# Kernel tuning notes

Hardware: AMD Instinct MI355X
Metric: run time of the kernel (lower is better)

Reference implementation:

```python
import jax, jax.numpy as jnp
import numpy as np

H, C_K, C_Q = 4, 512, 512


def setup_inputs() -> dict:
    key = jax.random.key(0)
    ks = jax.random.split(key, 6)
    s = 1.0 / np.sqrt(512.0)
    return {
        "x_k": jax.random.normal(ks[0], (4096, 512), jnp.float32),
        "x_q": jax.random.normal(ks[1], (4096, 512), jnp.float32),
        "k_w": jax.random.normal(ks[2], (H * C_K, 512), jnp.float32) * s,
        "q_w": jax.random.normal(ks[3], (H * C_Q, 512), jnp.float32) * s,
        "attn_w": jax.random.normal(ks[4], (H, C_K, C_Q), jnp.float32) * s,
        "proj_w": jax.random.normal(ks[5], (C_K, C_Q), jnp.float32) * s,
    }


def reference(x_k, x_q, k_w, q_w, attn_w, proj_w):
    # Project keys/queries and split into heads: [H, N, c]
    xk = (x_k @ k_w.T).reshape(-1, H, C_K).transpose(1, 0, 2)
    xq = (x_q @ q_w.T).reshape(-1, H, C_Q).transpose(1, 0, 2)
    # Bilinear scores: alphas[h, n, m] = xk[h,n,:] @ attn_w[h] @ xq[h,m,:]
    alphas = jnp.einsum("hnk,hkq,hmq->hnm", xk, attn_w, xq)
    # key-side update
    alpha_ks = jax.nn.softmax(alphas, axis=2)                 # [H, Nk, Nq]
    alpha_k_agg = jnp.mean(jnp.einsum("hnm,hmq->hnq", alpha_ks, xq), axis=0)
    x_k_update = alpha_k_agg @ proj_w.T                       # [Nk, C_K]
    # query-side update (bidirectional)
    alpha_qs = jax.nn.softmax(alphas.transpose(0, 2, 1), axis=2)  # [H, Nq, Nk]
    alpha_q_agg = jnp.mean(jnp.einsum("hmn,hnk->hmk", alpha_qs, xk), axis=0)
    x_q_update = alpha_q_agg @ proj_w                         # [Nq, C_Q]
    return x_k + x_k_update, x_q + x_q_update
```

## Files before the change

kernel.cpp:

```cpp
#include <hip/hip_runtime.h>
#include <stdint.h>

#define DEVI __device__ __forceinline__

typedef unsigned short u16;
typedef unsigned int u32;
typedef __attribute__((ext_vector_type(4))) unsigned short u16x4;
typedef __attribute__((ext_vector_type(8))) unsigned short u16x8;
typedef __attribute__((ext_vector_type(4))) float f32x4;
typedef __attribute__((ext_vector_type(8))) _Float16 f16x8;

static constexpr int NT = 4096;
static constexpr int D  = 512;
static constexpr int NH = 4;
static constexpr int KS = 4;

DEVI u16 f2h(float f) {
  _Float16 h = (_Float16)f;
  union { _Float16 h; u16 u; } v; v.h = h;
  return v.u;
}
DEVI float h2f(u16 u) {
  union { u16 u; _Float16 h; } v; v.u = u;
  return (float)v.h;
}

DEVI u32 enc_ord(float f) {
  u32 u = __float_as_uint(f);
  return (u & 0x80000000u) ? ~u : (u | 0x80000000u);
}
DEVI float dec_ord(u32 k) {
  u32 u = (k & 0x80000000u) ? (k ^ 0x80000000u) : ~k;
  return __uint_as_float(u);
}

DEVI void gld_lds16(const u16* g, u16* l) {
  __builtin_amdgcn_global_load_lds((const __attribute__((address_space(1))) void*)g,
                                   (__attribute__((address_space(3))) void*)l, 16, 0, 0);
}

enum { OUT_F32 = 0, OUT_F16 = 2, OUT_RES = 3, OUT_SMAX = 4, OUT_F16T = 5 };

template<int OUT>
__global__ __launch_bounds__(256)
void gemm_bt(const u16* __restrict__ A, int lda, size_t zsA,
             const u16* __restrict__ B, int ldb, size_t zsB,
             void* __restrict__ Cp, int ldc, size_t zsC,
             const float* __restrict__ res, const float* __restrict__ res2, int K,
             u32* __restrict__ rmg, u32* __restrict__ cmg,
             u16* __restrict__ STp, int ldct, size_t zsT)
{
  constexpr bool DOT = (OUT == OUT_SMAX || OUT == OUT_F16T);
  __shared__ u16 As[128 * 32];
  __shared__ u16 Bs[128 * 32];
  __shared__ u32 rmaxs[128], cmaxs[128];
  __shared__ u16 Tt[DOT ? 128 * 72 : 8];
  A += blockIdx.z * zsA;
  B += blockIdx.z * zsB;
  const float* resz = (OUT == OUT_RES && blockIdx.z) ? res2 : res;
  const int tid = threadIdx.x;
  const int lane = tid & 63, w = tid >> 6;
  const int wr = w >> 1, wc = w & 1;
  const int m0 = blockIdx.y * 128, n0 = blockIdx.x * 128;

  if (OUT == OUT_SMAX && tid < 128) { rmaxs[tid] = 0u; cmaxs[tid] = 0u; }

  f32x4 acc[4][4] = {};

  for (int k0 = 0; k0 < K; k0 += 32) {
    __syncthreads();
#pragma unroll
    for (int p = 0; p < 2; ++p) {
      int id = p * 256 + tid;
      int row = id >> 2, q = id & 3;
      gld_lds16(A + (size_t)(m0 + row) * lda + k0 + q * 8, As + id * 8);
      gld_lds16(B + (size_t)(n0 + row) * ldb + k0 + q * 8, Bs + id * 8);
    }
    __syncthreads();
    f16x8 af[4], bfv[4];
#pragma unroll
    for (int i = 0; i < 4; ++i)
      af[i] = *(const f16x8*)(As + (wr * 64 + i * 16 + (lane & 15)) * 32 + (lane >> 4) * 8);
#pragma unroll
    for (int i = 0; i < 4; ++i)
      bfv[i] = *(const f16x8*)(Bs + (wc * 64 + i * 16 + (lane & 15)) * 32 + (lane >> 4) * 8);
#pragma unroll
    for (int i = 0; i < 4; ++i)
#pragma unroll
      for (int j = 0; j < 4; ++j)
        acc[i][j] = __builtin_amdgcn_mfma_f32_16x16x32_f16(af[i], bfv[j], acc[i][j], 0, 0, 0);
  }

#pragma unroll
  for (int i = 0; i < 4; ++i) {
    int rl0 = wr * 64 + i * 16 + (lane >> 4) * 4;
#pragma unroll
    for (int j = 0; j < 4; ++j) {
      int c = n0 + wc * 64 + j * 16 + (lane & 15);
#pragma unroll
      for (int e = 0; e < 4; ++e) {
        size_t idx = blockIdx.z * zsC + (size_t)(m0 + rl0 + e) * ldc + c;
        float v = acc[i][j][e];
        if (OUT == OUT_F32) ((float*)Cp)[idx] = v;
        if (OUT == OUT_F16 || DOT) ((u16*)Cp)[idx] = f2h(v);
        if (OUT == OUT_RES) ((float*)Cp)[idx] = resz[(size_t)(m0 + rl0 + e) * ldc + c] + v;
      }
    }
  }

  if (OUT == OUT_SMAX) {
#pragma unroll
    for (int i = 0; i < 4; ++i) {
      int rl0 = wr * 64 + i * 16 + (lane >> 4) * 4;
#pragma unroll
      for (int e = 0; e < 4; ++e) {
        float m = fmaxf(fmaxf(acc[i][0][e], acc[i][1][e]), fmaxf(acc[i][2][e], acc[i][3][e]));
        atomicMax(&rmaxs[rl0 + e], enc_ord(m));
      }
    }
#pragma unroll
    for (int j = 0; j < 4; ++j) {
      float m = -3e38f;
#pragma unroll
      for (int i = 0; i < 4; ++i)
#pragma unroll
        for (int e = 0; e < 4; ++e) m = fmaxf(m, acc[i][j][e]);
      atomicMax(&cmaxs[wc * 64 + j * 16 + (lane & 15)], enc_ord(m));
    }
    __syncthreads();
    if (tid < 128) {
      atomicMax(rmg + m0 + tid, rmaxs[tid]);
      atomicMax(cmg + n0 + tid, cmaxs[tid]);
    }
  }

  if (DOT) {
#pragma unroll
    for (int half = 0; half < 2; ++half) {
      __syncthreads();
      if (wr == half) {
#pragma unroll
        for (int i = 0; i < 4; ++i) {
          int rl = i * 16 + (lane >> 4) * 4;
#pragma unroll
          for (int j = 0; j < 4; ++j) {
            int cl = wc * 64 + j * 16 + (lane & 15);
            u16x4 v;
            v[0] = f2h(acc[i][j][0]); v[1] = f2h(acc[i][j][1]);
            v[2] = f2h(acc[i][j][2]); v[3] = f2h(acc[i][j][3]);
            *(u16x4*)&Tt[cl * 72 + rl] = v;
          }
        }
      }
      __syncthreads();
#pragma unroll
      for (int q = 0; q < 4; ++q) {
        int id2 = q * 256 + tid;
        int c = id2 >> 3, mm = (id2 & 7) * 8;
        u16x8 v = *(const u16x8*)&Tt[c * 72 + mm];
        *(u16x8*)(STp + blockIdx.z * zsT + (size_t)(n0 + c) * ldct + m0 + half * 64 + mm) = v;
      }
    }
  }
}

__global__ __launch_bounds__(256)
void pv2(const u16* __restrict__ S, const u16* __restrict__ ST,
         const u32* __restrict__ rowm_u, const u32* __restrict__ colm_u,
         const u16* __restrict__ BQ, const u16* __restrict__ BK,
         u16* __restrict__ partK, u16* __restrict__ partQ,
         float* __restrict__ lk, float* __restrict__ lq, int Ksl)
{
  __shared__ u16 As[64 * 40];
  __shared__ u16 Bs[128 * 32];
  __shared__ float ps[4][64];
  __shared__ u16 lds_pad[10240];
  const int tid = threadIdx.x;
  const int lane = tid & 63, w = tid >> 6;
  const int wr = w >> 1, wc = w & 1;
  if (Ksl == 0) lds_pad[tid] = 0;

  const int lid = blockIdx.x + 4 * (blockIdx.y + 64 * blockIdx.z);
  const int swz = (lid & 7) * 128 + ((lid >> 3) & 127) + (lid >> 10) * 1024;
  const int bx = swz & 3, by = (swz >> 2) & 63, bz = (swz >> 8) & 3;
  const int dir = swz >> 10;

  const u16* Sarg = dir ? ST : S;
  const u32* mx_u = dir ? colm_u : rowm_u;
  const u16* B    = dir ? BK : BQ;
  u16* part       = dir ? partQ : partK;
  float* lpart    = dir ? lq : lk;

  const int m0 = by * 64, n0 = bx * 128;
  const int kb = bz * Ksl;

  const int rA = tid >> 2, kc = (tid & 3) * 8;
  const float mxA = dec_ord(mx_u[m0 + rA]);
  const u16* S0 = Sarg + (size_t)(m0 + rA) * NT + kb + kc;

  f32x4 acc[2][4] = {};
  float sacc = 0.f;

  f16x8 sv0 = *(const f16x8*)S0;

  for (int k0 = 0; k0 < Ksl; k0 += 32) {
    __syncthreads();
#pragma unroll
    for (int p = 0; p < 2; ++p) {
      int id = p * 256 + tid;
      int row = id >> 2, q = id & 3;
      gld_lds16(B + (size_t)(n0 + row) * NT + kb + k0 + q * 8, Bs + id * 8);
    }
    f16x8 nx0;
    if (k0 + 32 < Ksl) nx0 = *(const f16x8*)(S0 + k0 + 32);
    {
      u16x8 pk;
      float rs = 0.f;
#pragma unroll
      for (int j = 0; j < 8; ++j) {
        float e = __expf((float)sv0[j] - mxA);
        rs += e; pk[j] = f2h(e);
      }
      *(u16x8*)(As + rA * 40 + kc) = pk;
      sacc += rs;
    }
    __syncthreads();
    f16x8 af[2], bfv[4];
#pragma unroll
    for (int i = 0; i < 2; ++i)
      af[i] = *(const f16x8*)(As + (wr * 32 + i * 16 + (lane & 15)) * 40 + (lane >> 4) * 8);
#pragma unroll
    for (int j = 0; j < 4; ++j)
      bfv[j] = *(const f16x8*)(Bs + (wc * 64 + j * 16 + (lane & 15)) * 32 + (lane >> 4) * 8);
#pragma unroll
    for (int i = 0; i < 2; ++i)
#pragma unroll
      for (int j = 0; j < 4; ++j)
        acc[i][j] = __builtin_amdgcn_mfma_f32_16x16x32_f16(af[i], bfv[j], acc[i][j], 0, 0, 0);
    sv0 = nx0;
  }

  u16* out = part + (size_t)bz * NT * D;
#pragma unroll
  for (int i = 0; i < 2; ++i) {
    int r0 = m0 + wr * 32 + i * 16 + (lane >> 4) * 4;
#pragma unroll
    for (int j = 0; j < 4; ++j) {
      int c = n0 + wc * 64 + j * 16 + (lane & 15);
#pragma unroll
      for (int e = 0; e < 4; ++e)
        out[(size_t)(r0 + e) * D + c] = f2h(acc[i][j][e]);
    }
  }

  __syncthreads();
  ps[tid & 3][tid >> 2] = sacc;
  __syncthreads();
  if (bx == 0 && tid < 64) {
    lpart[(size_t)bz * NT + m0 + tid] =
        ps[0][tid] + ps[1][tid] + ps[2][tid] + ps[3][tid];
  }
}

__global__ __launch_bounds__(256)
void reduce2(const u16* __restrict__ pk, const float* __restrict__ lk,
             const u16* __restrict__ pq, const float* __restrict__ lq,
             u16* __restrict__ a0h, u16* __restrict__ a1h)
{
  const size_t i = ((size_t)blockIdx.x * 256 + threadIdx.x) * 4;
  const int m = (int)(i >> 9);
  const size_t zs = (size_t)NT * D;
  float Lk = 0.f, Lq = 0.f;
#pragma unroll
  for (int z = 0; z < KS; ++z) { Lk += lk[(size_t)z * NT + m]; Lq += lq[(size_t)z * NT + m]; }
  float s0 = 0.f, s1 = 0.f, s2 = 0.f, s3 = 0.f;
#pragma unroll
  for (int z = 0; z < KS; ++z) {
    u16x4 v = *(const u16x4*)(pk + z * zs + i);
    s0 += h2f(v[0]); s1 += h2f(v[1]); s2 += h2f(v[2]); s3 += h2f(v[3]);
  }
  float ck = 0.25f / Lk;
  u16x4 a = *(const u16x4*)(a0h + i);
  u16x4 na;
  na[0] = f2h(h2f(a[0]) + s0 * ck); na[1] = f2h(h2f(a[1]) + s1 * ck);
  na[2] = f2h(h2f(a[2]) + s2 * ck); na[3] = f2h(h2f(a[3]) + s3 * ck);
  *(u16x4*)(a0h + i) = na;
  s0 = s1 = s2 = s3 = 0.f;
#pragma unroll
  for (int z = 0; z < KS; ++z) {
    u16x4 v = *(const u16x4*)(pq + z * zs + i);
    s0 += h2f(v[0]); s1 += h2f(v[1]); s2 += h2f(v[2]); s3 += h2f(v[3]);
  }
  float cq = 0.25f / Lq;
  u16x4 b = *(const u16x4*)(a1h + i);
  u16x4 nb;
  nb[0] = f2h(h2f(b[0]) + s0 * cq); nb[1] = f2h(h2f(b[1]) + s1 * cq);
  nb[2] = f2h(h2f(b[2]) + s2 * cq); nb[3] = f2h(h2f(b[3]) + s3 * cq);
  *(u16x4*)(a1h + i) = nb;
}

__global__ __launch_bounds__(256)
void cast_multi(const float* p0, const float* p1, const float* p2,
                const float* p3, const float* p4, const float* p5,
                u16* o0, u16* o1, u16* o2, u16* o3, u16* o4, u16* o5,
                int n0, int n1, int n2, int n3, int n4, int n5)
{
  const float* in; u16* out; int n;
  switch (blockIdx.z) {
    case 0: in = p0; out = o0; n = n0; break;
    case 1: in = p1; out = o1; n = n1; break;
    case 2: in = p2; out = o2; n = n2; break;
    case 3: in = p3; out = o3; n = n3; break;
    case 4: in = p4; out = o4; n = n4; break;
    default: in = p5; out = o5; n = n5; break;
  }
  int i = (blockIdx.x * 256 + threadIdx.x) * 8;
  if (i >= n) return;
  f32x4 a = *(const f32x4*)(in + i), b = *(const f32x4*)(in + i + 4);
  u16x8 s;
  s[0] = f2h(a[0]); s[1] = f2h(a[1]); s[2] = f2h(a[2]); s[3] = f2h(a[3]);
  s[4] = f2h(b[0]); s[5] = f2h(b[1]); s[6] = f2h(b[2]); s[7] = f2h(b[3]);
  *(u16x8*)(out + i) = s;
}

__global__ __launch_bounds__(256)
void transpose_cast_f32(const float* __restrict__ in, int ldi,
                        u16* __restrict__ out, int ldo)
{
  __shared__ u16 t[64][72];
  int r0 = blockIdx.x * 64, c0 = blockIdx.y * 64;
  int t8 = threadIdx.x & 7, rr = threadIdx.x >> 3;
#pragma unroll
  for (int p = 0; p < 2; ++p) {
    int r = rr + p * 32;
    const float* src = in + (size_t)(r0 + r) * ldi + c0 + t8 * 8;
    f32x4 a = *(const f32x4*)src, b = *(const f32x4*)(src + 4);
    u16x8 s;
    s[0] = f2h(a[0]); s[1] = f2h(a[1]); s[2] = f2h(a[2]); s[3] = f2h(a[3]);
    s[4] = f2h(b[0]); s[5] = f2h(b[1]); s[6] = f2h(b[2]); s[7] = f2h(b[3]);
    *(u16x8*)&t[r][t8 * 8] = s;
  }
  __syncthreads();
#pragma unroll
  for (int p = 0; p < 2; ++p) {
    int c = rr + p * 32;
    u16x8 s;
#pragma unroll
    for (int j = 0; j < 8; ++j) s[j] = t[t8 * 8 + j][c];
    *(u16x8*)(out + (size_t)(c0 + c) * ldo + r0 + t8 * 8) = s;
  }
}

extern "C" void kernel_launch(void* const* d_in, const int* in_sizes, int n_in,
                              void* d_out, int out_size, void* d_ws, size_t ws_size,
                              hipStream_t stream)
{
  const float* x_k    = (const float*)d_in[0];
  const float* x_q    = (const float*)d_in[1];
  const float* k_w    = (const float*)d_in[2];
  const float* q_w    = (const float*)d_in[3];
  const float* attn_w = (const float*)d_in[4];
  const float* proj_w = (const float*)d_in[5];
  float* out0 = (float*)d_out;
  float* out1 = out0 + (size_t)NT * D;

  char* wptr = (char*)d_ws;
  auto alloc = [&](size_t bytes) { char* p = wptr; wptr += (bytes + 255) & ~(size_t)255; return p; };
  u16*   pb     = (u16*)  alloc((size_t)D * D * 2);
  u16*   pbT    = (u16*)  alloc((size_t)D * D * 2);
  u16*   XKall  = (u16*)  alloc((size_t)NT * NH * D * 2);
  u16*   XKTall = (u16*)  alloc((size_t)NT * NH * D * 2);
  u16*   XQTall = (u16*)  alloc((size_t)NT * NH * D * 2);
  u16*   Kpall  = (u16*)  alloc((size_t)NH * NT * D * 2);
  u16*   partK  = (u16*)  alloc((size_t)KS * NT * D * 2);
  u16*   partQ  = (u16*)  alloc((size_t)KS * NT * D * 2);
  u16*   agg0h  = (u16*)  alloc((size_t)NT * D * 2);
  u16*   agg1h  = (u16*)  alloc((size_t)NT * D * 2);
  float* lk     = (float*)alloc((size_t)KS * NT * 4);
  float* lq     = (float*)alloc((size_t)KS * NT * 4);
  u32*   rowm_u = (u32*)  alloc((size_t)NH * NT * 4);
  u32*   colm_u = (u32*)  alloc((size_t)NH * NT * 4);
  u16*   ST     = (u16*)  alloc((size_t)NT * NT * 2);
  char*  Sreg   = alloc((size_t)NT * NT * 2);
  u16*   S      = (u16*)Sreg;
  char* sp = Sreg;
  auto salloc = [&](size_t bytes) { char* p = sp; sp += (bytes + 255) & ~(size_t)255; return p; };
  u16* xkb   = (u16*)salloc((size_t)NT * D * 2);
  u16* xqb   = (u16*)salloc((size_t)NT * D * 2);
  u16* kwb   = (u16*)salloc((size_t)NH * D * D * 2);
  u16* qwb   = (u16*)salloc((size_t)NH * D * D * 2);
  u16* Abf   = (u16*)salloc((size_t)NH * D * D * 2);
  u16* XQall = (u16*)salloc((size_t)NT * NH * D * 2);

  cast_multi<<<dim3(NT * D / 2048, 1, 6), 256, 0, stream>>>(
      x_k, x_q, k_w, q_w, attn_w, proj_w,
      xkb, xqb, kwb, qwb, Abf, pb,
      NT * D, NT * D, NH * D * D, NH * D * D, NH * D * D, D * D);
  transpose_cast_f32<<<dim3(D / 64, D / 64), 256, 0, stream>>>(proj_w, D, pbT, D);

  gemm_bt<OUT_F16T><<<dim3(NH * D / 128, NT / 128, 2), 256, 0, stream>>>(
      xkb, D, (size_t)(xqb - xkb), kwb, D, (size_t)(qwb - kwb),
      XKall, NH * D, (size_t)(XQall - XKall), nullptr, nullptr, D,
      nullptr, nullptr, XKTall, NT, (size_t)(XQTall - XKTall));
  gemm_bt<OUT_F16><<<dim3(D / 128, NT / 128, NH), 256, 0, stream>>>(
      XQall, NH * D, (size_t)D, Abf, D, (size_t)D * D, Kpall, D, (size_t)NT * D,
      nullptr, nullptr, D, nullptr, nullptr, nullptr, 0, 0);

  hipMemsetAsync(agg0h, 0, (size_t)2 * NT * D * 2, stream);
  hipMemsetAsync(rowm_u, 0, (size_t)2 * NH * NT * 4, stream);

  for (int h = 0; h < NH; ++h) {
    const u16* XKh  = XKall + (size_t)h * D;
    const u16* XKTh = XKTall + (size_t)h * D * NT;
    const u16* XQTh = XQTall + (size_t)h * D * NT;
    const u16* Kph  = Kpall + (size_t)h * NT * D;
    u32* rmh = rowm_u + (size_t)h * NT;
    u32* cmh = colm_u + (size_t)h * NT;

    gemm_bt<OUT_SMAX><<<dim3(NT / 128, NT / 128), 256, 0, stream>>>(
        XKh, NH * D, 0, Kph, D, 0, S, NT, 0, nullptr, nullptr, D,
        rmh, cmh, ST, NT, 0);

    pv2<<<dim3(D / 128, NT / 64, 2 * KS), 256, 0, stream>>>(
        S, ST, rmh, cmh, XQTh, XKTh, partK, partQ, lk, lq, NT / KS);

    reduce2<<<NT * D / 1024, 256, 0, stream>>>(partK, lk, partQ, lq, agg0h, agg1h);
  }

  gemm_bt<OUT_RES><<<dim3(D / 128, NT / 128, 2), 256, 0, stream>>>(
      agg0h, D, (size_t)(agg1h - agg0h), pb, D, (size_t)(pbT - pb),
      out0, D, (size_t)NT * D, x_k, x_q, D, nullptr, nullptr, nullptr, 0, 0);
}
```

Before: 540.8 us.

## Drop LDS transpose staging and padding, use packed fp16 conversion in exp loop

The transposed-score epilogue of the GEMM now writes 4-element fp16 vectors directly to global memory instead of staging through a padded LDS tile with two barrier rounds. This removes the Tt shared buffer, which lowers LDS use and may allow more resident blocks. In pv2, the artificial lds_pad allocation that was limiting occupancy is removed. The exp conversion now uses packed round-toward-zero fp16 conversions. The trade-offs are narrower, less coalesced global stores for the transpose, different rounding of probabilities, and more blocks contending for cache.

```diff
diff --git a/kernel.cpp b/kernel.cpp
--- a/kernel.cpp
+++ b/kernel.cpp
@@ -8,6 +8,7 @@
 typedef __attribute__((ext_vector_type(4))) unsigned short u16x4;
 typedef __attribute__((ext_vector_type(8))) unsigned short u16x8;
 typedef __attribute__((ext_vector_type(4))) float f32x4;
+typedef __attribute__((ext_vector_type(2))) __fp16 hf16x2;
 typedef __attribute__((ext_vector_type(8))) _Float16 f16x8;
 
 static constexpr int NT = 4096;
@@ -54,7 +55,6 @@
   __shared__ u16 As[128 * 32];
   __shared__ u16 Bs[128 * 32];
   __shared__ u32 rmaxs[128], cmaxs[128];
-  __shared__ u16 Tt[DOT ? 128 * 72 : 8];
   A += blockIdx.z * zsA;
   B += blockIdx.z * zsB;
   const float* resz = (OUT == OUT_RES && blockIdx.z) ? res2 : res;
@@ -108,6 +108,21 @@
     }
   }
 
+  if (DOT) {
+#pragma unroll
+    for (int i = 0; i < 4; ++i) {
+      int ml = m0 + wr * 64 + i * 16 + (lane >> 4) * 4;
+#pragma unroll
+      for (int j = 0; j < 4; ++j) {
+        int c = n0 + wc * 64 + j * 16 + (lane & 15);
+        u16x4 v;
+        v[0] = f2h(acc[i][j][0]); v[1] = f2h(acc[i][j][1]);
+        v[2] = f2h(acc[i][j][2]); v[3] = f2h(acc[i][j][3]);
+        *(u16x4*)(STp + blockIdx.z * zsT + (size_t)c * ldct + ml) = v;
+      }
+    }
+  }
+
   if (OUT == OUT_SMAX) {
 #pragma unroll
     for (int i = 0; i < 4; ++i) {
@@ -131,35 +146,6 @@
     if (tid < 128) {
       atomicMax(rmg + m0 + tid, rmaxs[tid]);
       atomicMax(cmg + n0 + tid, cmaxs[tid]);
-    }
-  }
-
-  if (DOT) {
-#pragma unroll
-    for (int half = 0; half < 2; ++half) {
-      __syncthreads();
-      if (wr == half) {
-#pragma unroll
-        for (int i = 0; i < 4; ++i) {
-          int rl = i * 16 + (lane >> 4) * 4;
-#pragma unroll
-          for (int j = 0; j < 4; ++j) {
-            int cl = wc * 64 + j * 16 + (lane & 15);
-            u16x4 v;
-            v[0] = f2h(acc[i][j][0]); v[1] = f2h(acc[i][j][1]);
-            v[2] = f2h(acc[i][j][2]); v[3] = f2h(acc[i][j][3]);
-            *(u16x4*)&Tt[cl * 72 + rl] = v;
-          }
-        }
-      }
-      __syncthreads();
-#pragma unroll
-      for (int q = 0; q < 4; ++q) {
-        int id2 = q * 256 + tid;
-        int c = id2 >> 3, mm = (id2 & 7) * 8;
-        u16x8 v = *(const u16x8*)&Tt[c * 72 + mm];
-        *(u16x8*)(STp + blockIdx.z * zsT + (size_t)(n0 + c) * ldct + m0 + half * 64 + mm) = v;
-      }
     }
   }
 }
@@ -174,11 +160,9 @@
   __shared__ u16 As[64 * 40];
   __shared__ u16 Bs[128 * 32];
   __shared__ float ps[4][64];
-  __shared__ u16 lds_pad[10240];
   const int tid = threadIdx.x;
   const int lane = tid & 63, w = tid >> 6;
   const int wr = w >> 1, wc = w & 1;
-  if (Ksl == 0) lds_pad[tid] = 0;
 
   const int lid = blockIdx.x + 4 * (blockIdx.y + 64 * blockIdx.z);
   const int swz = (lid & 7) * 128 + ((lid >> 3) & 127) + (lid >> 10) * 1024;
@@ -214,13 +198,18 @@
     f16x8 nx0;
     if (k0 + 32 < Ksl) nx0 = *(const f16x8*)(S0 + k0 + 32);
     {
+      float ev[8];
+      float rs = 0.f;
+#pragma unroll
+      for (int j = 0; j < 8; ++j) {
+        ev[j] = __expf((float)sv0[j] - mxA);
+        rs += ev[j];
+      }
       u16x8 pk;
-      float rs = 0.f;
-#pragma unroll
-      for (int j = 0; j < 8; ++j) {
-        float e = __expf((float)sv0[j] - mxA);
-        rs += e; pk[j] = f2h(e);
-      }
+      ((hf16x2*)&pk)[0] = __builtin_amdgcn_cvt_pkrtz(ev[0], ev[1]);
+      ((hf16x2*)&pk)[1] = __builtin_amdgcn_cvt_pkrtz(ev[2], ev[3]);
+      ((hf16x2*)&pk)[2] = __builtin_amdgcn_cvt_pkrtz(ev[4], ev[5]);
+      ((hf16x2*)&pk)[3] = __builtin_amdgcn_cvt_pkrtz(ev[6], ev[7]);
       *(u16x8*)(As + rA * 40 + kc) = pk;
       sacc += rs;
     }
```

Measured after the change: 544.3 us. Within noise of the previous version (+0.6%).
